# Kernel optimization log

Hardware: AMD Instinct MI355X
Metric: run time of the kernel (lower is better)

Reference implementation:

```python
import jax, jax.numpy as jnp
import numpy as np

N = 50000      # nodes
E = 800000     # edges
H = 128        # hidden_features
EF = 8         # edge_features (before distance concat)
L = 2          # num_layers
NF = 100.0     # normalization_factor
NC = 1.0       # norm_constant
ATTN = True
USE_TANH = False
TANH_RANGE = 15.0
EIN = 2 * H + EF + 1  # GCL / coord-MLP edge input dim


def setup_inputs() -> dict:
    key = jax.random.key(0)
    ks = jax.random.split(key, 16)
    s = 0.02
    w = lambda k, shape: (jax.random.normal(k, shape, jnp.float32) * s)
    return dict(
        x=jax.random.normal(ks[0], (N, H), jnp.float32),
        pos=jax.random.normal(ks[1], (N, 3), jnp.float32),
        mask=jnp.ones((N, 1), jnp.float32),
        edge_attr=jax.random.normal(ks[2], (E, EF), jnp.float32),
        edge_index=jax.random.randint(ks[3], (2, E), 0, N),
        # GCL layer params, stacked over L layers
        W_e1=w(ks[4], (L, EIN, H)), b_e1=jnp.zeros((L, H), jnp.float32),
        W_e2=w(ks[5], (L, H, H)),  b_e2=jnp.zeros((L, H), jnp.float32),
        W_att=w(ks[6], (L, H, 1)), b_att=jnp.zeros((L, 1), jnp.float32),
        W_n1=w(ks[7], (L, 2 * H, H)), b_n1=jnp.zeros((L, H), jnp.float32),
        W_n2=w(ks[8], (L, H, H)),  b_n2=jnp.zeros((L, H), jnp.float32),
        # Equivariant coordinate-update MLP (last layer has no bias)
        cW1=w(ks[9], (EIN, H)), cb1=jnp.zeros((H,), jnp.float32),
        cW2=w(ks[10], (H, H)), cb2=jnp.zeros((H,), jnp.float32),
        cW3=w(ks[11], (H, 1)),
    )


def reference(x, pos, mask, edge_attr, edge_index,
              W_e1, b_e1, W_e2, b_e2, W_att, b_att, W_n1, b_n1, W_n2, b_n2,
              cW1, cb1, cW2, cb2, cW3):
    silu = jax.nn.silu
    row, col = edge_index[0], edge_index[1]  # aggregate messages at row
    diff = pos[row] - pos[col]                         # [E, 3]
    d2 = jnp.sum(diff * diff, axis=-1, keepdims=True)  # [E, 1] squared distance
    ea = jnp.concatenate([d2, edge_attr], axis=-1)     # [E, EF+1]

    # GCL message-passing layers (residual node update)
    for l in range(L):
        he = jnp.concatenate([x[row], x[col], ea], axis=-1)   # [E, EIN]
        m = silu(silu(he @ W_e1[l] + b_e1[l]) @ W_e2[l] + b_e2[l])
        if ATTN:
            m = m * jax.nn.sigmoid(m @ W_att[l] + b_att[l])
        agg = jax.ops.segment_sum(m, row, num_segments=N) / NF
        x = x + silu(jnp.concatenate([x, agg], axis=-1) @ W_n1[l] + b_n1[l]) @ W_n2[l] + b_n2[l]

    # Equivariant coordinate update
    he = jnp.concatenate([x[row], x[col], ea], axis=-1)
    phi = silu(silu(he @ cW1 + cb1) @ cW2 + cb2) @ cW3        # [E, 1]
    if USE_TANH:
        phi = jnp.tanh(phi) * TANH_RANGE
    nd = diff / (jnp.sqrt(d2) + NC)                           # normalized direction
    trans = nd * phi                                          # [E, 3]
    pos = pos + (jax.ops.segment_sum(trans, row, num_segments=N) / NF) * mask
    return (x, pos)
```

## Files before the change

kernel.cpp:

```cpp
#include <hip/hip_runtime.h>
#include <hip/hip_bf16.h>
#include <stdint.h>

#define NN 50000
#define NE 800000
#define HH 128

typedef __bf16 bf16x8 __attribute__((ext_vector_type(8)));
typedef float  f32x4  __attribute__((ext_vector_type(4)));
typedef long   f8frag;

__device__ __forceinline__ unsigned short f2bf(float f) {
  union { float f; uint32_t u; } v; v.f = f;
  uint32_t r = v.u + 0x7FFFu + ((v.u >> 16) & 1u);
  return (unsigned short)(r >> 16);
}
__device__ __forceinline__ float b2f(unsigned short u) {
  union { float f; uint32_t u; } v; v.u = (uint32_t)u << 16; return v.f;
}
#if __has_builtin(__builtin_amdgcn_cvt_pk_bf16_f32)
typedef __bf16 bf16x2 __attribute__((ext_vector_type(2)));
__device__ __forceinline__ uint32_t pack2bf(float a, float b) {
  union { bf16x2 v; uint32_t u; } t;
  t.v = __builtin_amdgcn_cvt_pk_bf16_f32(a, b);
  return t.u;
}
#else
__device__ __forceinline__ uint32_t pack2bf(float a, float b) {
  return (uint32_t)f2bf(a) | ((uint32_t)f2bf(b) << 16);
}
#endif
__device__ __forceinline__ uint8_t f2fp8(float v) {
  return (uint8_t)(__builtin_amdgcn_cvt_pk_fp8_f32(v, 0.f, 0, false) & 0xff);
}
__device__ __forceinline__ float silu_f(float x) {
  return x * __builtin_amdgcn_rcpf(1.f + __expf(-x));
}
__device__ __forceinline__ float sigm_f(float x) {
  return __builtin_amdgcn_rcpf(1.f + __expf(-x));
}

__device__ __forceinline__ bf16x8 frag_ld(const short* blk, int row, int q) {
  int c = q ^ ((row >> 1) & 3);
  return *(const bf16x8*)(blk + row * 32 + c * 8);
}
__device__ __forceinline__ int wfrag_off(int row, int q) {
  return row * 32 + ((q ^ ((row >> 1) & 3)) * 8);
}
__device__ __forceinline__ bf16x8 fragf32(const float* src, float sc) {
  float4 lo = *(const float4*)src;
  float4 hi = *(const float4*)(src + 4);
  union { uint32_t u[4]; bf16x8 v; } t;
  t.u[0] = pack2bf(lo.x * sc, lo.y * sc);
  t.u[1] = pack2bf(lo.z * sc, lo.w * sc);
  t.u[2] = pack2bf(hi.x * sc, hi.y * sc);
  t.u[3] = pack2bf(hi.z * sc, hi.w * sc);
  return t.v;
}

__global__ void k_prep_weights(const float* We1, const float* We2, const float* Wn1,
                               const float* Wn2, const float* cW1, const float* cW2,
                               uint8_t* W1f8, short* W2sw, short* Wn1sw, short* Wn2sw,
                               short* W1csw) {
  int idx = blockIdx.x * 256 + threadIdx.x;
  if (idx < 110592) {
    int l = idx / 36864, rem = idx % 36864;
    const float* s = (l == 0) ? We1 : (l == 1) ? We1 + 33920 : cW1;
    int kkb = rem >> 12, r2 = rem & 4095;
    int n = r2 >> 5, kw = r2 & 31;
    int k = kkb * 32 + kw;
    float v = (k < 265) ? s[k * 128 + n] : 0.f;
    W1f8[idx] = f2fp8(v);
    return;
  }
  idx -= 110592;
  if (idx < 49152) {
    int l = idx >> 14, rem = idx & 16383;
    const float* s = (l == 0) ? We2 : (l == 1) ? We2 + 16384 : cW2;
    int kkb = rem >> 12, r2 = rem & 4095, n = r2 >> 5, kw = r2 & 31;
    int cp = kw >> 3, j = kw & 7, c = cp ^ ((n >> 1) & 3);
    int k = kkb * 32 + c * 8 + j;
    W2sw[(l << 14) + (rem)] = (short)f2bf(s[k * 128 + n]);
    return;
  }
  idx -= 49152;
  if (idx < 65536) {
    int l = idx >> 15, rem = idx & 32767;
    const float* s = Wn1 + l * 32768;
    int kkb = rem >> 12, r2 = rem & 4095, n = r2 >> 5, kw = r2 & 31;
    int cp = kw >> 3, j = kw & 7, c = cp ^ ((n >> 1) & 3);
    int k = kkb * 32 + c * 8 + j;
    Wn1sw[(l << 15) + rem] = (short)f2bf(s[k * 128 + n]);
    return;
  }
  idx -= 65536;
  if (idx < 32768) {
    int l = idx >> 14, rem = idx & 16383;
    const float* s = Wn2 + l * 16384;
    int kkb = rem >> 12, r2 = rem & 4095, n = r2 >> 5, kw = r2 & 31;
    int cp = kw >> 3, j = kw & 7, c = cp ^ ((n >> 1) & 3);
    int k = kkb * 32 + c * 8 + j;
    Wn2sw[(l << 14) + rem] = (short)f2bf(s[k * 128 + n]);
    return;
  }
  idx -= 32768;
  if (idx < 98304) {
    int l = idx / 32768, rem = idx % 32768;
    const float* s = (l == 0) ? We1 : (l == 1) ? We1 + 33920 : cW1;
    int kkb = rem >> 13, r2 = rem & 8191, n = r2 >> 5, kw = r2 & 31;
    int cp = kw >> 3, j = kw & 7, c = cp ^ ((n >> 1) & 3);
    int k = kkb * 32 + c * 8 + j;
    float v = (n < 128) ? s[k * 128 + n] : s[(128 + k) * 128 + (n - 128)];
    W1csw[l * 32768 + rem] = (short)f2bf(v);
  }
}

__global__ void k_edge_pre(const float* __restrict__ pos, const float* __restrict__ eattr,
                           const int* __restrict__ ei, const int* __restrict__ sortedIdx,
                           int* __restrict__ rowS, int* __restrict__ colS,
                           uint8_t* __restrict__ eaF8, float* __restrict__ ndS) {
  int p = blockIdx.x * 256 + threadIdx.x;
  if (p >= NE) return;
  int e = sortedIdx[p];
  int r = ei[e], c = ei[NE + e];
  float dx = pos[r * 3 + 0] - pos[c * 3 + 0];
  float dy = pos[r * 3 + 1] - pos[c * 3 + 1];
  float dz = pos[r * 3 + 2] - pos[c * 3 + 2];
  float d2 = dx * dx + dy * dy + dz * dz;
  float invd = __builtin_amdgcn_rcpf(sqrtf(d2) + 1.f);
  rowS[p] = r;
  colS[p] = c;
  ndS[p * 3 + 0] = dx * invd;
  ndS[p * 3 + 1] = dy * invd;
  ndS[p * 3 + 2] = dz * invd;
  const float* ea = eattr + (size_t)e * 8;
  uint32_t w0 = __builtin_amdgcn_cvt_pk_fp8_f32(d2, ea[0], 0, false);
  w0 = __builtin_amdgcn_cvt_pk_fp8_f32(ea[1], ea[2], w0, true);
  uint32_t w1 = __builtin_amdgcn_cvt_pk_fp8_f32(ea[3], ea[4], 0, false);
  w1 = __builtin_amdgcn_cvt_pk_fp8_f32(ea[5], ea[6], w1, true);
  uint32_t w2 = __builtin_amdgcn_cvt_pk_fp8_f32(ea[7], 0.f, 0, false);
  uint4 v = {w0, w1, w2, 0u};
  *(uint4*)(eaF8 + (size_t)p * 16) = v;
}
__global__ void k_pos_final(const float* __restrict__ pos, const float* __restrict__ mask,
                            const float* __restrict__ pagg, float* __restrict__ out) {
  int i = blockIdx.x * 256 + threadIdx.x;
  if (i < NN * 3) out[i] = pos[i] + pagg[i] * 0.01f * mask[i / 3];
}

__global__ void k_hist(const int* __restrict__ ei, int* __restrict__ cnt) {
  int e = blockIdx.x * 256 + threadIdx.x;
  if (e < NE) atomicAdd(&cnt[ei[e]], 1);
}
__global__ void k_scan_block(const int* __restrict__ cnt, int* __restrict__ offs,
                             int* __restrict__ bsum) {
  __shared__ int s[256];
  int i = blockIdx.x * 256 + threadIdx.x;
  int v = (i < NN) ? cnt[i] : 0;
  s[threadIdx.x] = v;
  __syncthreads();
#pragma unroll
  for (int d = 1; d < 256; d <<= 1) {
    int t = (threadIdx.x >= d) ? s[threadIdx.x - d] : 0;
    __syncthreads();
    s[threadIdx.x] += t;
    __syncthreads();
  }
  if (i < NN) offs[i] = s[threadIdx.x] - v;
  if (threadIdx.x == 255) bsum[blockIdx.x] = s[255];
}
__global__ void k_scan_top(int* __restrict__ bsum) {
  __shared__ int s[256];
  int v = (threadIdx.x < 196) ? bsum[threadIdx.x] : 0;
  s[threadIdx.x] = v;
  __syncthreads();
#pragma unroll
  for (int d = 1; d < 256; d <<= 1) {
    int t = (threadIdx.x >= d) ? s[threadIdx.x - d] : 0;
    __syncthreads();
    s[threadIdx.x] += t;
    __syncthreads();
  }
  if (threadIdx.x < 196) bsum[threadIdx.x] = s[threadIdx.x] - v;
}
__global__ void k_scan_add(int* __restrict__ offs, const int* __restrict__ bsum) {
  int i = blockIdx.x * 256 + threadIdx.x;
  if (i < NN) offs[i] += bsum[blockIdx.x];
}
__global__ void k_scatter(const int* __restrict__ ei, int* __restrict__ offs,
                          int* __restrict__ sortedIdx) {
  int e = blockIdx.x * 256 + threadIdx.x;
  if (e < NE) sortedIdx[atomicAdd(&offs[ei[e]], 1)] = e;
}

__global__ __launch_bounds__(256) void k_h1(
    const float* __restrict__ x, const short* __restrict__ W1c,
    const float* __restrict__ b1, short* __restrict__ H1RC,
    float* __restrict__ aggZ) {
  const int tid = threadIdx.x, lane = tid & 63, w = tid >> 6;
  const int ln = lane & 15, q = lane >> 4;
  const int tile = blockIdx.x;
  {
    float4* a4 = (float4*)aggZ;
    const float4 z4 = {0.f, 0.f, 0.f, 0.f};
#pragma unroll
    for (int k = 0; k < 8; ++k) {
      int i4 = tile * 2048 + k * 256 + tid;
      if (i4 < NN * 32) a4[i4] = z4;
    }
  }
  size_t nbase[4];
  int wofs[4];
#pragma unroll
  for (int i = 0; i < 4; ++i) {
    int node = tile * 64 + i * 16 + ln;
    nbase[i] = (size_t)(node < NN ? node : (NN - 1)) * 128;
    int row = w * 64 + i * 16 + ln;
    wofs[i] = row * 32 + ((q ^ ((row >> 1) & 3)) * 8);
  }
  f32x4 acc[4][4];
  const f32x4 zero4 = {0.f, 0.f, 0.f, 0.f};
#pragma unroll
  for (int mi = 0; mi < 4; ++mi)
#pragma unroll
    for (int ni = 0; ni < 4; ++ni) acc[mi][ni] = zero4;
#pragma unroll
  for (int kk = 0; kk < 4; ++kk) {
    bf16x8 af[4], bfr[4];
#pragma unroll
    for (int i = 0; i < 4; ++i) af[i] = fragf32(x + nbase[i] + kk * 32 + q * 8, 1.f);
#pragma unroll
    for (int i = 0; i < 4; ++i) bfr[i] = *(const bf16x8*)(W1c + kk * 8192 + wofs[i]);
#pragma unroll
    for (int mi = 0; mi < 4; ++mi)
#pragma unroll
      for (int ni = 0; ni < 4; ++ni)
        acc[mi][ni] = __builtin_amdgcn_mfma_f32_16x16x32_bf16(af[mi], bfr[ni], acc[mi][ni], 0, 0, 0);
  }
  float b1v[4];
#pragma unroll
  for (int ni = 0; ni < 4; ++ni) {
    int ch = w * 64 + ni * 16 + ln;
    b1v[ni] = (ch < 128) ? b1[ch] : 0.f;
  }
#pragma unroll
  for (int mi = 0; mi < 4; ++mi)
#pragma unroll
    for (int r = 0; r < 4; ++r) {
      int node = tile * 64 + mi * 16 + q * 4 + r;
      if (node < NN) {
        ushort4 pk;
        pk.x = f2bf(acc[mi][0][r] + b1v[0]);
        pk.y = f2bf(acc[mi][1][r] + b1v[1]);
        pk.z = f2bf(acc[mi][2][r] + b1v[2]);
        pk.w = f2bf(acc[mi][3][r] + b1v[3]);
        *(ushort4*)(H1RC + (size_t)node * 256 + w * 64 + ln * 4) = pk;
      }
    }
}

template <int COORD>
__global__ __launch_bounds__(256, 5) void k_edge_gemm(
    const short* __restrict__ H1RC, const uint8_t* __restrict__ eaF8,
    const int* __restrict__ rowS, const int* __restrict__ colS,
    const uint8_t* __restrict__ W1f8, const short* __restrict__ W2l,
    const float* __restrict__ b2,
    const float* __restrict__ wred, const float* __restrict__ batt,
    const float* __restrict__ ndS, float* outAcc) {
  __shared__ __align__(16) short A2s[8192];
  __shared__ float redp[64][2];
  __shared__ __align__(16) unsigned short attb[64];
  __shared__ int srow[64];
  __shared__ __align__(8) unsigned char srunS[64];
  __shared__ int runrowS[64];
  __shared__ int cntS[1];

  const int tid = threadIdx.x;
  const int lane = tid & 63;
  const int w = tid >> 6;
  const int ln = lane & 15, q = lane >> 4;
  const int wm = w >> 1, wn = w & 1;

  const int nwg = gridDim.x;
  const int qq = nwg >> 3, rr = nwg & 7;
  const int xcd = blockIdx.x & 7, bidx = blockIdx.x >> 3;
  const int tile = (xcd < rr ? xcd * (qq + 1) : rr * (qq + 1) + (xcd - rr) * qq) + bidx;
  const int ebase = tile * 64;

  bool is_start = false;
  if (w == 0) {
    int myrow = rowS[ebase + tid];
    srow[tid] = myrow;
    int prevrow = (tid > 0) ? rowS[ebase + tid - 1] : (myrow ^ 1);
    is_start = (tid == 0) || (myrow != prevrow);
    unsigned long long bmask = __ballot(is_start);
    if (tid == 0) cntS[0] = __popcll(bmask);
    int run = __popcll(bmask & ((1ull << lane) - 1ull)) + (is_start ? 1 : 0) - 1;
    srunS[tid] = (unsigned char)run;
    if (is_start) runrowS[run] = myrow;
  }

  const int e0 = wm * 32 + ln, e1 = e0 + 16;
  const uint32_t cbp = (uint32_t)(wn * 64 + q * 16);
  const uint32_t hr0 = (uint32_t)rowS[ebase + e0] * 256u + cbp;
  const uint32_t hr1 = (uint32_t)rowS[ebase + e1] * 256u + cbp;
  const uint32_t hc0 = (uint32_t)colS[ebase + e0] * 256u + 128u + cbp;
  const uint32_t hc1 = (uint32_t)colS[ebase + e1] * 256u + 128u + cbp;
  const uint32_t ea0 = (uint32_t)(ebase + e0) * 16u + (uint32_t)((q & 1) * 8);
  const uint32_t ea1 = (uint32_t)(ebase + e1) * 16u + (uint32_t)((q & 1) * 8);
  int wofs8[4], wofs[4];
#pragma unroll
  for (int i = 0; i < 4; ++i) {
    wofs8[i] = (wn * 64 + i * 16 + ln) * 32 + q * 8;
    wofs[i] = wfrag_off(wn * 64 + i * 16 + ln, q);
  }

  union U8 { uint4 v; unsigned short s[8]; };
  U8 xr[2][2], xc[2][2];
  xr[0][0].v = *(const uint4*)(H1RC + hr0);
  xr[0][1].v = *(const uint4*)(H1RC + hr0 + 8);
  xr[1][0].v = *(const uint4*)(H1RC + hr1);
  xr[1][1].v = *(const uint4*)(H1RC + hr1 + 8);
  xc[0][0].v = *(const uint4*)(H1RC + hc0);
  xc[0][1].v = *(const uint4*)(H1RC + hc0 + 8);
  xc[1][0].v = *(const uint4*)(H1RC + hc1);
  xc[1][1].v = *(const uint4*)(H1RC + hc1 + 8);

  f32x4 acc[4][2];
  const f32x4 zero4 = {0.f, 0.f, 0.f, 0.f};
#pragma unroll
  for (int ni = 0; ni < 4; ++ni)
#pragma unroll
    for (int mi = 0; mi < 2; ++mi) acc[ni][mi] = zero4;

  {
    const uint8_t* W1ea = W1f8 + 8 * 4096;
    f8frag wf[4], hf[2];
#pragma unroll
    for (int i = 0; i < 4; ++i) wf[i] = *(const f8frag*)(W1ea + wofs8[i]);
    hf[0] = (q < 2) ? *(const f8frag*)(eaF8 + ea0) : 0L;
    hf[1] = (q < 2) ? *(const f8frag*)(eaF8 + ea1) : 0L;
#pragma unroll
    for (int ni = 0; ni < 4; ++ni)
#pragma unroll
      for (int mi = 0; mi < 2; ++mi)
        acc[ni][mi] = __builtin_amdgcn_mfma_f32_16x16x32_fp8_fp8(wf[ni], hf[mi], acc[ni][mi], 0, 0, 0);
  }

#pragma unroll
  for (int ni = 0; ni < 4; ++ni) {
    int cb = wn * 64 + ni * 16 + q * 4;
    int kkb = cb >> 5, cc = (cb >> 3) & 3, j0 = cb & 7;
#pragma unroll
    for (int mi = 0; mi < 2; ++mi) {
      int edge = wm * 32 + mi * 16 + ln;
      int addr = kkb * 2048 + edge * 32 + ((cc ^ ((edge >> 1) & 3)) * 8) + j0;
      float h0 = silu_f(acc[ni][mi][0] + b2f(xr[mi][0].s[ni]) + b2f(xc[mi][0].s[ni]));
      float h1 = silu_f(acc[ni][mi][1] + b2f(xr[mi][0].s[4 + ni]) + b2f(xc[mi][0].s[4 + ni]));
      float h2 = silu_f(acc[ni][mi][2] + b2f(xr[mi][1].s[ni]) + b2f(xc[mi][1].s[ni]));
      float h3 = silu_f(acc[ni][mi][3] + b2f(xr[mi][1].s[4 + ni]) + b2f(xc[mi][1].s[4 + ni]));
      uint2 pk;
      pk.x = pack2bf(h0, h1);
      pk.y = pack2bf(h2, h3);
      *(uint2*)(A2s + addr) = pk;
    }
  }
  __syncthreads();

  f32x4 acc2[4][2];
#pragma unroll
  for (int ni = 0; ni < 4; ++ni)
#pragma unroll
    for (int mi = 0; mi < 2; ++mi) acc2[ni][mi] = zero4;
#pragma unroll
  for (int kk = 0; kk < 4; ++kk) {
    bf16x8 wf[4], hf[2];
#pragma unroll
    for (int i = 0; i < 4; ++i) wf[i] = *(const bf16x8*)(W2l + kk * 4096 + wofs[i]);
#pragma unroll
    for (int i = 0; i < 2; ++i) hf[i] = frag_ld(A2s + kk * 2048, wm * 32 + i * 16 + ln, q);
#pragma unroll
    for (int ni = 0; ni < 4; ++ni)
#pragma unroll
      for (int mi = 0; mi < 2; ++mi)
        acc2[ni][mi] = __builtin_amdgcn_mfma_f32_16x16x32_bf16(wf[ni], hf[mi], acc2[ni][mi], 0, 0, 0);
  }

  float4 b2v[4], wv[4];
#pragma unroll
  for (int ni = 0; ni < 4; ++ni) {
    b2v[ni] = *(const float4*)(b2 + wn * 64 + ni * 16 + q * 4);
    wv[ni]  = *(const float4*)(wred + wn * 64 + ni * 16 + q * 4);
  }
  float p[2] = {0.f, 0.f};
#pragma unroll
  for (int ni = 0; ni < 4; ++ni)
#pragma unroll
    for (int mi = 0; mi < 2; ++mi)
#pragma unroll
      for (int r = 0; r < 4; ++r) {
        float v = silu_f(acc2[ni][mi][r] + ((const float*)&b2v[ni])[r]);
        acc2[ni][mi][r] = v;
        p[mi] += v * ((const float*)&wv[ni])[r];
      }
#pragma unroll
  for (int mi = 0; mi < 2; ++mi) {
    p[mi] += __shfl_xor(p[mi], 16, 64);
    p[mi] += __shfl_xor(p[mi], 32, 64);
  }
  if (lane < 16) {
#pragma unroll
    for (int mi = 0; mi < 2; ++mi) redp[wm * 32 + mi * 16 + ln][wn] = p[mi];
  }
  __syncthreads();

  if (COORD == 0) {
    if (tid < 64) attb[tid] = f2bf(sigm_f(redp[tid][0] + redp[tid][1] + batt[0]));
#pragma unroll
    for (int ni = 0; ni < 4; ++ni)
#pragma unroll
      for (int mi = 0; mi < 2; ++mi) {
        int eb = mi * 16 + ln;
        int cE = (eb >> 3) & 3, jE = eb & 7;
#pragma unroll
        for (int r = 0; r < 4; ++r) {
          int chan2 = wn * 64 + ni * 16 + q * 4 + r;
          int addr = wm * 4096 + chan2 * 32 + ((cE ^ ((chan2 >> 1) & 3)) * 8) + jE;
          union { float f; uint32_t u; } vv;
          vv.f = acc2[ni][mi][r];
          A2s[addr] = (short)((vv.u + 0x8000u) >> 16);
        }
      }
    __syncthreads();
    const int nruns = cntS[0];
    bf16x8 bfrg[2][2];
#pragma unroll
    for (int kk = 0; kk < 2; ++kk)
#pragma unroll
      for (int ni = 0; ni < 2; ++ni)
        bfrg[kk][ni] = frag_ld(A2s + kk * 4096, w * 32 + ni * 16 + ln, q);
    const int npass = (nruns + 15) >> 4;
    for (int pp = 0; pp < npass; ++pp) {
      const unsigned int base = pp * 16;
      f32x4 a3c[2] = {zero4, zero4};
#pragma unroll
      for (int kk = 0; kk < 2; ++kk) {
        uint2 sb = *(const uint2*)(srunS + kk * 32 + q * 8);
        U8 ab;
        ab.v = *(const uint4*)(attb + kk * 32 + q * 8);
        union { short s[8]; bf16x8 v; } af;
#pragma unroll
        for (int j = 0; j < 4; ++j)
          af.s[j] = (((sb.x >> (8 * j)) & 255u) == base + (unsigned)ln) ? (short)ab.s[j] : (short)0;
#pragma unroll
        for (int j = 0; j < 4; ++j)
          af.s[4 + j] = (((sb.y >> (8 * j)) & 255u) == base + (unsigned)ln) ? (short)ab.s[4 + j] : (short)0;
        a3c[0] = __builtin_amdgcn_mfma_f32_16x16x32_bf16(af.v, bfrg[kk][0], a3c[0], 0, 0, 0);
        a3c[1] = __builtin_amdgcn_mfma_f32_16x16x32_bf16(af.v, bfrg[kk][1], a3c[1], 0, 0, 0);
      }
#pragma unroll
      for (int ni = 0; ni < 2; ++ni)
#pragma unroll
        for (int r = 0; r < 4; ++r) {
          int run = (int)base + q * 4 + r;
          if (run < nruns) {
            int rw = runrowS[run];
            atomicAdd(&outAcc[(size_t)rw * 128 + (w * 32 + ni * 16 + ln)], a3c[ni][r]);
          }
        }
    }
  } else {
    float* ndl = (float*)A2s;
    if (tid < 64) {
      float phi = redp[tid][0] + redp[tid][1];
      ndl[tid * 3 + 0] = ndS[(size_t)(ebase + tid) * 3 + 0] * phi;
      ndl[tid * 3 + 1] = ndS[(size_t)(ebase + tid) * 3 + 1] * phi;
      ndl[tid * 3 + 2] = ndS[(size_t)(ebase + tid) * 3 + 2] * phi;
    }
    __syncthreads();
    if (is_start) {
      int myrow = srow[tid];
      float s0 = 0.f, s1 = 0.f, s2 = 0.f;
      for (int j = tid; j < 64 && srow[j] == myrow; ++j) {
        s0 += ndl[j * 3 + 0];
        s1 += ndl[j * 3 + 1];
        s2 += ndl[j * 3 + 2];
      }
      atomicAdd(&outAcc[myrow * 3 + 0], s0);
      atomicAdd(&outAcc[myrow * 3 + 1], s1);
      atomicAdd(&outAcc[myrow * 3 + 2], s2);
    }
  }
}

__global__ __launch_bounds__(256) void k_node_gemm(
    const float* __restrict__ agg,
    const short* __restrict__ Wn1l, const short* __restrict__ Wn2l,
    const float* __restrict__ b1, const float* __restrict__ b2,
    const float* __restrict__ xres, float* __restrict__ xout,
    const short* __restrict__ W1cN, const float* __restrict__ b1N,
    short* __restrict__ H1RC, float* __restrict__ aggZ) {
  __shared__ short A2s[4 * 2048];

  const int tid = threadIdx.x;
  const int lane = tid & 63;
  const int w = tid >> 6;
  const int ln = lane & 15, q = lane >> 4;
  const int wm = w >> 1, wn = w & 1;
  const int tile = blockIdx.x;

  size_t nbase[2];
  int wofs[4];
#pragma unroll
  for (int i = 0; i < 2; ++i) {
    int node = tile * 64 + wm * 32 + i * 16 + ln;
    nbase[i] = (size_t)(node < NN ? node : (NN - 1)) * 128;
  }
#pragma unroll
  for (int i = 0; i < 4; ++i) wofs[i] = wfrag_off(wn * 64 + i * 16 + ln, q);

  f32x4 acc[2][4];
  const f32x4 zero4 = {0.f, 0.f, 0.f, 0.f};
#pragma unroll
  for (int mi = 0; mi < 2; ++mi)
#pragma unroll
    for (int ni = 0; ni < 4; ++ni) acc[mi][ni] = zero4;

#pragma unroll
  for (int kk = 0; kk < 8; ++kk) {
    bf16x8 af[2], bfr[4];
#pragma unroll
    for (int i = 0; i < 2; ++i) {
      if (kk < 4) af[i] = fragf32(xres + nbase[i] + kk * 32 + q * 8, 1.f);
      else        af[i] = fragf32(agg + nbase[i] + (kk - 4) * 32 + q * 8, 0.01f);
    }
#pragma unroll
    for (int i = 0; i < 4; ++i) bfr[i] = *(const bf16x8*)(Wn1l + kk * 4096 + wofs[i]);
#pragma unroll
    for (int mi = 0; mi < 2; ++mi)
#pragma unroll
      for (int ni = 0; ni < 4; ++ni)
        acc[mi][ni] = __builtin_amdgcn_mfma_f32_16x16x32_bf16(af[mi], bfr[ni], acc[mi][ni], 0, 0, 0);
  }

  if (aggZ) {
    float4* a4 = (float4*)aggZ;
    const float4 z4 = {0.f, 0.f, 0.f, 0.f};
#pragma unroll
    for (int k = 0; k < 8; ++k) {
      int i4 = tile * 2048 + k * 256 + tid;
      if (i4 < NN * 32) a4[i4] = z4;
    }
  }

  float b1v[4];
#pragma unroll
  for (int ni = 0; ni < 4; ++ni) b1v[ni] = b1[wn * 64 + ni * 16 + ln];
#pragma unroll
  for (int mi = 0; mi < 2; ++mi)
#pragma unroll
    for (int ni = 0; ni < 4; ++ni) {
      int chan = wn * 64 + ni * 16 + ln;
      int kkb = chan >> 5, c = (chan >> 3) & 3, jj = chan & 7;
#pragma unroll
      for (int r = 0; r < 4; ++r) {
        int m = wm * 32 + mi * 16 + q * 4 + r;
        float v = silu_f(acc[mi][ni][r] + b1v[ni]);
        A2s[kkb * 2048 + m * 32 + ((c ^ ((m >> 1) & 3)) * 8) + jj] = (short)f2bf(v);
      }
    }
  __syncthreads();

  f32x4 acc2[2][4];
#pragma unroll
  for (int mi = 0; mi < 2; ++mi)
#pragma unroll
    for (int ni = 0; ni < 4; ++ni) acc2[mi][ni] = zero4;
#pragma unroll
  for (int kk = 0; kk < 4; ++kk) {
    bf16x8 af[2], bfr[4];
#pragma unroll
    for (int i = 0; i < 2; ++i) af[i] = frag_ld(A2s + kk * 2048, wm * 32 + i * 16 + ln, q);
#pragma unroll
    for (int i = 0; i < 4; ++i) bfr[i] = *(const bf16x8*)(Wn2l + kk * 4096 + wofs[i]);
#pragma unroll
    for (int mi = 0; mi < 2; ++mi)
#pragma unroll
      for (int ni = 0; ni < 4; ++ni)
        acc2[mi][ni] = __builtin_amdgcn_mfma_f32_16x16x32_bf16(af[mi], bfr[ni], acc2[mi][ni], 0, 0, 0);
  }

  float b2v[4];
#pragma unroll
  for (int ni = 0; ni < 4; ++ni) b2v[ni] = b2[wn * 64 + ni * 16 + ln];
#pragma unroll
  for (int mi = 0; mi < 2; ++mi)
#pragma unroll
    for (int r = 0; r < 4; ++r) {
      int m = wm * 32 + mi * 16 + q * 4 + r;
      int node = tile * 64 + m;
      if (node < NN) {
#pragma unroll
        for (int ni = 0; ni < 4; ++ni) {
          int chan = wn * 64 + ni * 16 + ln;
          float v = acc2[mi][ni][r] + b2v[ni] + xres[(size_t)node * 128 + chan];
          acc2[mi][ni][r] = v;
          xout[(size_t)node * 128 + chan] = v;
        }
      }
    }

  __syncthreads();
#pragma unroll
  for (int mi = 0; mi < 2; ++mi)
#pragma unroll
    for (int ni = 0; ni < 4; ++ni) {
      int chan = wn * 64 + ni * 16 + ln;
      int kkb = chan >> 5, c = (chan >> 3) & 3, jj = chan & 7;
#pragma unroll
      for (int r = 0; r < 4; ++r) {
        int m = wm * 32 + mi * 16 + q * 4 + r;
        A2s[kkb * 2048 + m * 32 + ((c ^ ((m >> 1) & 3)) * 8) + jj] = (short)f2bf(acc2[mi][ni][r]);
      }
    }
  __syncthreads();

  int wofsH[4];
#pragma unroll
  for (int i = 0; i < 4; ++i) {
    int row = w * 64 + i * 16 + ln;
    wofsH[i] = row * 32 + ((q ^ ((row >> 1) & 3)) * 8);
  }
  f32x4 acc3[4][4];
#pragma unroll
  for (int mi = 0; mi < 4; ++mi)
#pragma unroll
    for (int ni = 0; ni < 4; ++ni) acc3[mi][ni] = zero4;
#pragma unroll
  for (int kk = 0; kk < 4; ++kk) {
    bf16x8 af[4], bfr[4];
#pragma unroll
    for (int i = 0; i < 4; ++i) af[i] = frag_ld(A2s + kk * 2048, i * 16 + ln, q);
#pragma unroll
    for (int i = 0; i < 4; ++i) bfr[i] = *(const bf16x8*)(W1cN + kk * 8192 + wofsH[i]);
#pragma unroll
    for (int mi = 0; mi < 4; ++mi)
#pragma unroll
      for (int ni = 0; ni < 4; ++ni)
        acc3[mi][ni] = __builtin_amdgcn_mfma_f32_16x16x32_bf16(af[mi], bfr[ni], acc3[mi][ni], 0, 0, 0);
  }
  float b1v2[4];
#pragma unroll
  for (int ni = 0; ni < 4; ++ni) {
    int ch = w * 64 + ni * 16 + ln;
    b1v2[ni] = (ch < 128) ? b1N[ch] : 0.f;
  }
#pragma unroll
  for (int mi = 0; mi < 4; ++mi)
#pragma unroll
    for (int r = 0; r < 4; ++r) {
      int node = tile * 64 + mi * 16 + q * 4 + r;
      if (node < NN) {
        ushort4 pk;
        pk.x = f2bf(acc3[mi][0][r] + b1v2[0]);
        pk.y = f2bf(acc3[mi][1][r] + b1v2[1]);
        pk.z = f2bf(acc3[mi][2][r] + b1v2[2]);
        pk.w = f2bf(acc3[mi][3][r] + b1v2[3]);
        *(ushort4*)(H1RC + (size_t)node * 256 + w * 64 + ln * 4) = pk;
      }
    }
}

extern "C" void kernel_launch(void* const* d_in, const int* in_sizes, int n_in,
                              void* d_out, int out_size, void* d_ws, size_t ws_size,
                              hipStream_t stream) {
  const float* x    = (const float*)d_in[0];
  const float* pos  = (const float*)d_in[1];
  const float* mask = (const float*)d_in[2];
  const float* eattr= (const float*)d_in[3];
  const int*   ei   = (const int*)d_in[4];
  const float* We1  = (const float*)d_in[5];
  const float* be1  = (const float*)d_in[6];
  const float* We2  = (const float*)d_in[7];
  const float* be2  = (const float*)d_in[8];
  const float* Watt = (const float*)d_in[9];
  const float* batt = (const float*)d_in[10];
  const float* Wn1  = (const float*)d_in[11];
  const float* bn1  = (const float*)d_in[12];
  const float* Wn2  = (const float*)d_in[13];
  const float* bn2  = (const float*)d_in[14];
  const float* cW1  = (const float*)d_in[15];
  const float* cb1  = (const float*)d_in[16];
  const float* cW2  = (const float*)d_in[17];
  const float* cb2  = (const float*)d_in[18];
  const float* cW3  = (const float*)d_in[19];

  char* p = (char*)d_ws;
  auto carve = [&](size_t bytes) { char* r = p; p += (bytes + 511) & ~(size_t)511; return r; };
  short*   H1RC  = (short*)carve((size_t)NN * 256 * 2);
  uint8_t* eaF8  = (uint8_t*)carve((size_t)NE * 16 + 256);
  int*     rowS  = (int*)carve((size_t)NE * 4);
  int*     colS  = (int*)carve((size_t)NE * 4);
  float*   ndS   = (float*)carve((size_t)NE * 3 * 4);
  float*   agg   = (float*)carve((size_t)NN * 128 * 4);
  float*   xcur  = (float*)carve((size_t)NN * 128 * 4);
  float*   pagg  = (float*)carve((size_t)NN * 3 * 4);
  uint8_t* W1f8  = (uint8_t*)carve(3 * 36864);
  short*   W2sw  = (short*)carve(3 * 16384 * 2);
  short*   Wn1sw = (short*)carve(2 * 32768 * 2);
  short*   Wn2sw = (short*)carve(2 * 16384 * 2);
  short*   W1csw = (short*)carve(3 * 32768 * 2);
  int*     cnt   = (int*)carve((size_t)NN * 4);
  int*     offs  = (int*)carve((size_t)NN * 4);
  int*     bsum  = (int*)carve(256 * 4);
  int*     sortedIdx = (int*)carve((size_t)NE * 4);

  float* xout_f = (float*)d_out;
  float* pout_f = xout_f + NN * 128;

  k_prep_weights<<<1392, 256, 0, stream>>>(We1, We2, Wn1, Wn2, cW1, cW2,
                                           W1f8, W2sw, Wn1sw, Wn2sw, W1csw);

  hipMemsetAsync(cnt, 0, (size_t)NN * 4, stream);
  k_hist<<<3125, 256, 0, stream>>>(ei, cnt);
  k_scan_block<<<196, 256, 0, stream>>>(cnt, offs, bsum);
  k_scan_top<<<1, 256, 0, stream>>>(bsum);
  k_scan_add<<<196, 256, 0, stream>>>(offs, bsum);
  k_scatter<<<3125, 256, 0, stream>>>(ei, offs, sortedIdx);
  k_edge_pre<<<3125, 256, 0, stream>>>(pos, eattr, ei, sortedIdx, rowS, colS, eaF8, ndS);

  k_h1<<<782, 256, 0, stream>>>(x, W1csw, be1, H1RC, agg);

  k_edge_gemm<0><<<12500, 256, 0, stream>>>(H1RC, eaF8, rowS, colS,
      W1f8, W2sw, be2, Watt, batt, (const float*)nullptr, agg);
  k_node_gemm<<<782, 256, 0, stream>>>(agg, Wn1sw, Wn2sw, bn1, bn2,
      x, xcur, W1csw + 32768, be1 + 128, H1RC, agg);

  k_edge_gemm<0><<<12500, 256, 0, stream>>>(H1RC, eaF8, rowS, colS,
      W1f8 + 36864, W2sw + 16384, be2 + 128, Watt + 128, batt + 1,
      (const float*)nullptr, agg);
  k_node_gemm<<<782, 256, 0, stream>>>(agg, Wn1sw + 32768, Wn2sw + 16384,
      bn1 + 128, bn2 + 128, xcur, xout_f, W1csw + 2 * 32768, cb1, H1RC,
      (float*)nullptr);

  hipMemsetAsync(pagg, 0, (size_t)NN * 3 * 4, stream);
  k_edge_gemm<1><<<12500, 256, 0, stream>>>(H1RC, eaF8, rowS, colS,
      W1f8 + 2 * 36864, W2sw + 2 * 16384, cb2, cW3, (const float*)nullptr, ndS, pagg);
  k_pos_final<<<587, 256, 0, stream>>>(pos, mask, pagg, pout_f);
}
```

Before: 705.2 us.

## Merge setup kernels, fold scan-add into scatter, skip atomics for interior runs

Merges weight prep with the histogram, and node-h1 with the scatter, so fewer launches are needed. The scan-add pass is removed by adding the block sum inside the scatter. The pagg memset moves into edge_pre, and acc2 reuses the acc registers. Row runs that lie entirely inside one edge tile are now written with plain stores instead of atomics. This is only correct if no other tile touches those rows, which holds because edges are sorted by row.

Result: no change. 712.7 us (+1.1%).

```diff
diff --git a/kernel.cpp b/kernel.cpp
--- a/kernel.cpp
+++ b/kernel.cpp
@@ -58,11 +58,11 @@
   return t.v;
 }
 
-__global__ void k_prep_weights(const float* We1, const float* We2, const float* Wn1,
-                               const float* Wn2, const float* cW1, const float* cW2,
-                               uint8_t* W1f8, short* W2sw, short* Wn1sw, short* Wn2sw,
-                               short* W1csw) {
-  int idx = blockIdx.x * 256 + threadIdx.x;
+__device__ void prep_weights_body(int idx, const float* We1, const float* We2,
+                                  const float* Wn1, const float* Wn2,
+                                  const float* cW1, const float* cW2,
+                                  uint8_t* W1f8, short* W2sw, short* Wn1sw,
+                                  short* Wn2sw, short* W1csw) {
   if (idx < 110592) {
     int l = idx / 36864, rem = idx % 36864;
     const float* s = (l == 0) ? We1 : (l == 1) ? We1 + 33920 : cW1;
@@ -115,11 +115,27 @@
   }
 }
 
+__global__ void k_setup1(const float* We1, const float* We2, const float* Wn1,
+                         const float* Wn2, const float* cW1, const float* cW2,
+                         uint8_t* W1f8, short* W2sw, short* Wn1sw, short* Wn2sw,
+                         short* W1csw, const int* __restrict__ ei,
+                         int* __restrict__ cnt) {
+  if (blockIdx.x < 1392) {
+    prep_weights_body(blockIdx.x * 256 + threadIdx.x, We1, We2, Wn1, Wn2, cW1, cW2,
+                      W1f8, W2sw, Wn1sw, Wn2sw, W1csw);
+  } else {
+    int e = (blockIdx.x - 1392) * 256 + threadIdx.x;
+    if (e < NE) atomicAdd(&cnt[ei[e]], 1);
+  }
+}
+
 __global__ void k_edge_pre(const float* __restrict__ pos, const float* __restrict__ eattr,
                            const int* __restrict__ ei, const int* __restrict__ sortedIdx,
                            int* __restrict__ rowS, int* __restrict__ colS,
-                           uint8_t* __restrict__ eaF8, float* __restrict__ ndS) {
+                           uint8_t* __restrict__ eaF8, float* __restrict__ ndS,
+                           float* __restrict__ pagg) {
   int p = blockIdx.x * 256 + threadIdx.x;
+  if (p < NN * 3) pagg[p] = 0.f;
   if (p >= NE) return;
   int e = sortedIdx[p];
   int r = ei[e], c = ei[NE + e];
@@ -148,10 +164,6 @@
   if (i < NN * 3) out[i] = pos[i] + pagg[i] * 0.01f * mask[i / 3];
 }
 
-__global__ void k_hist(const int* __restrict__ ei, int* __restrict__ cnt) {
-  int e = blockIdx.x * 256 + threadIdx.x;
-  if (e < NE) atomicAdd(&cnt[ei[e]], 1);
-}
 __global__ void k_scan_block(const int* __restrict__ cnt, int* __restrict__ offs,
                              int* __restrict__ bsum) {
   __shared__ int s[256];
@@ -183,23 +195,12 @@
   }
   if (threadIdx.x < 196) bsum[threadIdx.x] = s[threadIdx.x] - v;
 }
-__global__ void k_scan_add(int* __restrict__ offs, const int* __restrict__ bsum) {
-  int i = blockIdx.x * 256 + threadIdx.x;
-  if (i < NN) offs[i] += bsum[blockIdx.x];
-}
-__global__ void k_scatter(const int* __restrict__ ei, int* __restrict__ offs,
-                          int* __restrict__ sortedIdx) {
-  int e = blockIdx.x * 256 + threadIdx.x;
-  if (e < NE) sortedIdx[atomicAdd(&offs[ei[e]], 1)] = e;
-}
-
-__global__ __launch_bounds__(256) void k_h1(
-    const float* __restrict__ x, const short* __restrict__ W1c,
-    const float* __restrict__ b1, short* __restrict__ H1RC,
-    float* __restrict__ aggZ) {
-  const int tid = threadIdx.x, lane = tid & 63, w = tid >> 6;
+
+__device__ void h1_body(int tile, int tid, const float* __restrict__ x,
+                        const short* __restrict__ W1c, const float* __restrict__ b1,
+                        short* __restrict__ H1RC, float* __restrict__ aggZ) {
+  const int lane = tid & 63, w = tid >> 6;
   const int ln = lane & 15, q = lane >> 4;
-  const int tile = blockIdx.x;
   {
     float4* a4 = (float4*)aggZ;
     const float4 z4 = {0.f, 0.f, 0.f, 0.f};
@@ -257,6 +258,22 @@
         *(ushort4*)(H1RC + (size_t)node * 256 + w * 64 + ln * 4) = pk;
       }
     }
+}
+
+__global__ __launch_bounds__(256) void k_setup2(
+    const float* __restrict__ x, const short* __restrict__ W1c,
+    const float* __restrict__ b1, short* __restrict__ H1RC, float* __restrict__ aggZ,
+    const int* __restrict__ ei, int* __restrict__ offs, const int* __restrict__ bsum,
+    int* __restrict__ sortedIdx) {
+  if (blockIdx.x < 782) {
+    h1_body(blockIdx.x, threadIdx.x, x, W1c, b1, H1RC, aggZ);
+  } else {
+    int e = (blockIdx.x - 782) * 256 + threadIdx.x;
+    if (e < NE) {
+      int r = ei[e];
+      sortedIdx[atomicAdd(&offs[r], 1) + bsum[r >> 8]] = e;
+    }
+  }
 }
 
 template <int COORD>
@@ -367,11 +384,10 @@
   }
   __syncthreads();
 
-  f32x4 acc2[4][2];
 #pragma unroll
   for (int ni = 0; ni < 4; ++ni)
 #pragma unroll
-    for (int mi = 0; mi < 2; ++mi) acc2[ni][mi] = zero4;
+    for (int mi = 0; mi < 2; ++mi) acc[ni][mi] = zero4;
 #pragma unroll
   for (int kk = 0; kk < 4; ++kk) {
     bf16x8 wf[4], hf[2];
@@ -383,7 +399,7 @@
     for (int ni = 0; ni < 4; ++ni)
 #pragma unroll
       for (int mi = 0; mi < 2; ++mi)
-        acc2[ni][mi] = __builtin_amdgcn_mfma_f32_16x16x32_bf16(wf[ni], hf[mi], acc2[ni][mi], 0, 0, 0);
+        acc[ni][mi] = __builtin_amdgcn_mfma_f32_16x16x32_bf16(wf[ni], hf[mi], acc[ni][mi], 0, 0, 0);
   }
 
   float4 b2v[4], wv[4];
@@ -399,8 +415,8 @@
     for (int mi = 0; mi < 2; ++mi)
 #pragma unroll
       for (int r = 0; r < 4; ++r) {
-        float v = silu_f(acc2[ni][mi][r] + ((const float*)&b2v[ni])[r]);
-        acc2[ni][mi][r] = v;
+        float v = silu_f(acc[ni][mi][r] + ((const float*)&b2v[ni])[r]);
+        acc[ni][mi][r] = v;
         p[mi] += v * ((const float*)&wv[ni])[r];
       }
 #pragma unroll
@@ -427,7 +443,7 @@
           int chan2 = wn * 64 + ni * 16 + q * 4 + r;
           int addr = wm * 4096 + chan2 * 32 + ((cE ^ ((chan2 >> 1) & 3)) * 8) + jE;
           union { float f; uint32_t u; } vv;
-          vv.f = acc2[ni][mi][r];
+          vv.f = acc[ni][mi][r];
           A2s[addr] = (short)((vv.u + 0x8000u) >> 16);
         }
       }
@@ -465,7 +481,9 @@
           int run = (int)base + q * 4 + r;
           if (run < nruns) {
             int rw = runrowS[run];
-            atomicAdd(&outAcc[(size_t)rw * 128 + (w * 32 + ni * 16 + ln)], a3c[ni][r]);
+            float* dst = &outAcc[(size_t)rw * 128 + (w * 32 + ni * 16 + ln)];
+            if (run > 0 && run < nruns - 1) *dst = a3c[ni][r];
+            else atomicAdd(dst, a3c[ni][r]);
           }
         }
     }
@@ -481,14 +499,22 @@
     if (is_start) {
       int myrow = srow[tid];
       float s0 = 0.f, s1 = 0.f, s2 = 0.f;
-      for (int j = tid; j < 64 && srow[j] == myrow; ++j) {
+      int j = tid;
+      for (; j < 64 && srow[j] == myrow; ++j) {
         s0 += ndl[j * 3 + 0];
         s1 += ndl[j * 3 + 1];
         s2 += ndl[j * 3 + 2];
       }
-      atomicAdd(&outAcc[myrow * 3 + 0], s0);
-      atomicAdd(&outAcc[myrow * 3 + 1], s1);
-      atomicAdd(&outAcc[myrow * 3 + 2], s2);
+      bool excl = (tid > 0) && (j < 64);
+      if (excl) {
+        outAcc[myrow * 3 + 0] = s0;
+        outAcc[myrow * 3 + 1] = s1;
+        outAcc[myrow * 3 + 2] = s2;
+      } else {
+        atomicAdd(&outAcc[myrow * 3 + 0], s0);
+        atomicAdd(&outAcc[myrow * 3 + 1], s1);
+        atomicAdd(&outAcc[myrow * 3 + 2], s2);
+      }
     }
   }
 }
@@ -718,18 +744,15 @@
   float* xout_f = (float*)d_out;
   float* pout_f = xout_f + NN * 128;
 
-  k_prep_weights<<<1392, 256, 0, stream>>>(We1, We2, Wn1, Wn2, cW1, cW2,
-                                           W1f8, W2sw, Wn1sw, Wn2sw, W1csw);
-
   hipMemsetAsync(cnt, 0, (size_t)NN * 4, stream);
-  k_hist<<<3125, 256, 0, stream>>>(ei, cnt);
+  k_setup1<<<1392 + 3125, 256, 0, stream>>>(We1, We2, Wn1, Wn2, cW1, cW2,
+                                            W1f8, W2sw, Wn1sw, Wn2sw, W1csw, ei, cnt);
   k_scan_block<<<196, 256, 0, stream>>>(cnt, offs, bsum);
   k_scan_top<<<1, 256, 0, stream>>>(bsum);
-  k_scan_add<<<196, 256, 0, stream>>>(offs, bsum);
-  k_scatter<<<3125, 256, 0, stream>>>(ei, offs, sortedIdx);
-  k_edge_pre<<<3125, 256, 0, stream>>>(pos, eattr, ei, sortedIdx, rowS, colS, eaF8, ndS);
-
-  k_h1<<<782, 256, 0, stream>>>(x, W1csw, be1, H1RC, agg);
+  k_setup2<<<782 + 3125, 256, 0, stream>>>(x, W1csw, be1, H1RC, agg,
+                                           ei, offs, bsum, sortedIdx);
+  k_edge_pre<<<3125, 256, 0, stream>>>(pos, eattr, ei, sortedIdx,
+                                       rowS, colS, eaF8, ndS, pagg);
 
   k_edge_gemm<0><<<12500, 256, 0, stream>>>(H1RC, eaF8, rowS, colS,
       W1f8, W2sw, be2, Watt, batt, (const float*)nullptr, agg);
@@ -743,7 +766,6 @@
       bn1 + 128, bn2 + 128, xcur, xout_f, W1csw + 2 * 32768, cb1, H1RC,
       (float*)nullptr);
 
-  hipMemsetAsync(pagg, 0, (size_t)NN * 3 * 4, stream);
   k_edge_gemm<1><<<12500, 256, 0, stream>>>(H1RC, eaF8, rowS, colS,
       W1f8 + 2 * 36864, W2sw + 2 * 16384, cb2, cW3, (const float*)nullptr, ndS, pagg);
   k_pos_final<<<587, 256, 0, stream>>>(pos, mask, pagg, pout_f);
```
